# Optimization experiments

Hardware: AMD Instinct MI355X
Metric: run time of the kernel (lower is better)

Reference implementation:

```python
import jax, jax.numpy as jnp
import numpy as np

VOXEL_SIZE = 0.4
STRIDE = 2
NUM_BATCH = 4
PRE_MAXSIZE = 1024  # nms_premaxsize
NMS_THR = 0.1
NEG_INF = -1e9


def setup_inputs() -> dict:
    key = jax.random.key(0)
    ks = jax.random.split(key, 7)
    N, C = 200000, 256
    feat = jax.random.normal(ks[0], (N, C), dtype=jnp.float32)
    batch_idx = jax.random.randint(ks[1], (N,), 0, NUM_BATCH, dtype=jnp.int32)
    coor = jax.random.randint(ks[2], (N, 2), 0, 400, dtype=jnp.int32)
    W_cls = jax.random.normal(ks[3], (C, 2), dtype=jnp.float32) * 0.02
    b_cls = jnp.zeros((2,), dtype=jnp.float32)
    W_reg = jax.random.normal(ks[4], (C, 9), dtype=jnp.float32) * 0.02
    b_reg = jnp.zeros((9,), dtype=jnp.float32)
    return {"feat": feat, "batch_idx": batch_idx, "coor": coor,
            "W_cls": W_cls, "b_cls": b_cls, "W_reg": W_reg, "b_reg": b_reg}


def _bev_iou(bx):
    # bx: [K,7] (x,y,z,l,w,h,r); axis-aligned BEV IoU on (x,y,l,w)
    x, y, l, w = bx[:, 0], bx[:, 1], bx[:, 3], bx[:, 4]
    x1, x2 = x - l / 2, x + l / 2
    y1, y2 = y - w / 2, y + w / 2
    ix = jnp.maximum(jnp.minimum(x2[:, None], x2[None, :]) - jnp.maximum(x1[:, None], x1[None, :]), 0.0)
    iy = jnp.maximum(jnp.minimum(y2[:, None], y2[None, :]) - jnp.maximum(y1[:, None], y1[None, :]), 0.0)
    inter = ix * iy
    area = l * w
    union = area[:, None] + area[None, :] - inter
    return inter / jnp.maximum(union, 1e-6)


def _nms_keep(iou):
    # greedy NMS over score-descending rows; returns keep mask [K]
    K = iou.shape[0]
    idx = jnp.arange(K)

    def body(i, supp):
        keep_i = jnp.logical_not(supp[i])
        new = keep_i & (iou[i] > NMS_THR) & (idx > i)
        return supp | new

    supp = jax.lax.fori_loop(0, K, body, jnp.zeros((K,), dtype=bool))
    return jnp.logical_not(supp)


def reference(feat, batch_idx, coor, W_cls, b_cls, W_reg, b_reg):
    # ---- shared heads over all sparse voxels ----
    cls_logits = feat @ W_cls + b_cls            # [N, 1+1] (neg evidence, class)
    probs = jax.nn.softmax(cls_logits, axis=-1)
    cls_prob = probs[:, 1:]                      # [N, n_cls]
    conf = jnp.max(cls_prob, axis=-1)            # [N]
    label = jnp.argmax(cls_prob, axis=-1)        # [N]

    reg = feat @ W_reg + b_reg                   # [N, 9] -> ctr(3) dim(3) dir(2) scr(1)
    ctr, dim, drn, scr = reg[:, :3], reg[:, 3:6], reg[:, 6:8], reg[:, 8]
    scr = jax.nn.sigmoid(scr)                    # sigmoid_keys=['scr']

    # indices2metric: voxel indices -> metric centers
    centers = coor.astype(jnp.float32) * (VOXEL_SIZE * STRIDE)  # [N, 2]

    xy = centers + ctr[:, :2]
    z = ctr[:, 2]
    lwh = jnp.exp(jnp.clip(dim, -6.0, 6.0))
    angle = jnp.arctan2(drn[:, 0], drn[:, 1])
    boxes = jnp.concatenate([xy, z[:, None], lwh, angle[:, None]], axis=-1)  # [N, 7]
    score = conf * scr                           # [N]

    def per_sample(b):
        s = jnp.where(batch_idx == b, score, NEG_INF)
        vals, idx = jax.lax.top_k(s, PRE_MAXSIZE)          # score-sorted (desc)
        bx = boxes[idx]                                     # [K, 7]
        lb = label[idx]                                     # [K]
        valid = vals > NEG_INF / 2
        iou = _bev_iou(bx)
        keep = _nms_keep(iou) & valid
        out = jnp.concatenate([bx, vals[:, None]], axis=-1) * keep[:, None]  # [K, 8]
        return out, lb, keep

    out, lb, keep = jax.vmap(per_sample)(jnp.arange(NUM_BATCH))
    return out, lb, keep
```

## Files before the change

kernel.cpp:

```cpp
#include <hip/hip_runtime.h>
#include <math.h>

#define NBATCH 4
#define PRE 1024
#define CAND 4096
#define NHIST 65536
#define MAXSLOT 384

__device__ __forceinline__ unsigned long long allow_mask(int i, int l) {
    int base = l << 6;
    if (i < base) return ~0ull;
    int sh = i - base + 1;
    if (sh >= 64) return 0ull;
    return (~0ull) << sh;
}

__global__ void k0_weights(const float* __restrict__ Wcls, const float* __restrict__ bcls,
                           const float* __restrict__ Wreg, const float* __restrict__ breg,
                           double* __restrict__ Wd3, float* __restrict__ Wf8,
                           double* __restrict__ biasD, float* __restrict__ biasF) {
    int j = blockIdx.x;
    int c = threadIdx.x;
    if (j < 2) {
        Wd3[j * 256 + c] = (double)Wcls[c * 2 + j];
        if (c == 0) biasD[j] = (double)bcls[j];
    } else if (j == 10) {
        Wd3[2 * 256 + c] = (double)Wreg[c * 9 + 8];
        if (c == 0) biasD[2] = (double)breg[8];
    } else {
        int r = j - 2;
        Wf8[r * 256 + c] = Wreg[c * 9 + r];
        if (c == 0) biasF[r] = breg[r];
    }
}

__global__ __launch_bounds__(256, 4) void k1_points(
    const float4* __restrict__ feat4, const int* __restrict__ batch_idx,
    const int* __restrict__ coor, const double* __restrict__ Wd3,
    const float* __restrict__ Wf8, const double* __restrict__ biasD,
    const float* __restrict__ biasF, float* __restrict__ pointData,
    unsigned long long* __restrict__ keys, unsigned int* __restrict__ hist, int N) {
    int p = blockIdx.x * 256 + threadIdx.x;
    int pc = (p < N) ? p : 0;
    const float4* row = feat4 + (size_t)pc * 64;

    double a0 = 0.0, a1 = 0.0, a2 = 0.0;
    float f[8] = {0.f, 0.f, 0.f, 0.f, 0.f, 0.f, 0.f, 0.f};
    float4 cur[8], nxt[8];
#pragma unroll
    for (int u = 0; u < 8; ++u) cur[u] = row[u];
#pragma unroll
    for (int o = 0; o < 8; ++o) {
        if (o < 7) {
#pragma unroll
            for (int u = 0; u < 8; ++u) nxt[u] = row[(o + 1) * 8 + u];
        }
#pragma unroll
        for (int u = 0; u < 8; ++u) {
            float vv[4] = {cur[u].x, cur[u].y, cur[u].z, cur[u].w};
#pragma unroll
            for (int m = 0; m < 4; ++m) {
                int k = o * 32 + u * 4 + m;
                double fd = (double)vv[m];
                a0 = fma(fd, Wd3[k], a0);
                a1 = fma(fd, Wd3[256 + k], a1);
                a2 = fma(fd, Wd3[512 + k], a2);
#pragma unroll
                for (int j = 0; j < 8; ++j) f[j] = fmaf(vv[m], Wf8[j * 256 + k], f[j]);
            }
        }
#pragma unroll
        for (int u = 0; u < 8; ++u) cur[u] = nxt[u];
    }
    if (p >= N) return;

    double d0 = a0 + biasD[0], d1 = a1 + biasD[1], d2 = a2 + biasD[2];
    double conf = 1.0 / (1.0 + exp(-(d1 - d0)));
    double scr = 1.0 / (1.0 + exp(-d2));
    double score = conf * scr;
    float s32 = (float)score;

    float fb[8];
#pragma unroll
    for (int j = 0; j < 8; ++j) fb[j] = f[j] + biasF[j];

    float cx = (float)coor[2 * p] * 0.8f;
    float cy = (float)coor[2 * p + 1] * 0.8f;
    float bx = cx + fb[0], by = cy + fb[1], bz = fb[2];
    float bl = expf(fminf(fmaxf(fb[3], -6.f), 6.f));
    float bw = expf(fminf(fmaxf(fb[4], -6.f), 6.f));
    float bh = expf(fminf(fmaxf(fb[5], -6.f), 6.f));
    float ba = atan2f(fb[6], fb[7]);

    float4* pd = (float4*)(pointData + (size_t)p * 8);
    pd[0] = make_float4(bx, by, bz, bl);
    pd[1] = make_float4(bw, bh, ba, s32);
    keys[p] = (unsigned long long)__double_as_longlong(score);
    int b = batch_idx[p];
    atomicAdd(&hist[b * NHIST + (__float_as_uint(s32) >> 16)], 1u);
}

__global__ __launch_bounds__(256) void k2_thresh(const unsigned int* __restrict__ hist,
                                                 unsigned int* __restrict__ Tarr,
                                                 unsigned int* __restrict__ candCount) {
    int b = blockIdx.x, tid = threadIdx.x;
    __shared__ unsigned int csum[256];
    __shared__ unsigned int chunkv[256];
    __shared__ int stc;
    __shared__ unsigned int scum;
    if (tid == 0) candCount[b] = 0u;
    const unsigned int* h = hist + b * NHIST;
    unsigned int s = 0;
    for (int m = 0; m < 256; ++m) s += h[tid * 256 + m];
    csum[tid] = s;
    __syncthreads();
    if (tid == 0) {
        unsigned int cum = 0; int tc = -1;
        for (int t = 255; t >= 0; --t) {
            if (cum + csum[t] >= 1024u) { tc = t; break; }
            cum += csum[t];
        }
        stc = tc; scum = cum;
    }
    __syncthreads();
    int tc = stc;
    if (tc < 0) { if (tid == 0) Tarr[b] = 0u; return; }
    chunkv[tid] = h[tc * 256 + tid];
    __syncthreads();
    if (tid == 0) {
        unsigned int cum = scum, T = (unsigned int)(tc * 256);
        for (int m = 255; m >= 0; --m) {
            unsigned int c = chunkv[m];
            if (cum + c >= 1024u) { T = (unsigned int)(tc * 256 + m); break; }
            cum += c;
        }
        Tarr[b] = T;
    }
}

__global__ void k3_compact(const int* __restrict__ batch_idx, const float* __restrict__ pointData,
                           const unsigned long long* __restrict__ keys,
                           const unsigned int* __restrict__ Tarr, unsigned int* __restrict__ candCount,
                           unsigned int* __restrict__ candIdx, unsigned long long* __restrict__ candKey,
                           int N) {
    int p = blockIdx.x * 256 + threadIdx.x;
    if (p >= N) return;
    int b = batch_idx[p];
    float s32 = pointData[(size_t)p * 8 + 7];
    unsigned int bucket = __float_as_uint(s32) >> 16;
    if (bucket >= Tarr[b]) {
        unsigned int pos = atomicAdd(&candCount[b], 1u);
        if (pos < CAND) {
            candIdx[b * CAND + pos] = (unsigned int)p;
            candKey[b * CAND + pos] = keys[p];
        }
    }
}

__global__ __launch_bounds__(1024) void k4_sort(const unsigned int* __restrict__ candCount,
                                                const unsigned int* __restrict__ candIdx,
                                                const unsigned long long* __restrict__ candKey,
                                                const float* __restrict__ pointData,
                                                float* __restrict__ topBox,
                                                float4* __restrict__ geo,
                                                unsigned int* __restrict__ validArr) {
    int b = blockIdx.x, tid = threadIdx.x;
    __shared__ unsigned long long ka[CAND];
    __shared__ unsigned int id[CAND];
    unsigned int cnt = candCount[b];
    if (cnt > CAND) cnt = CAND;
    int n = (cnt <= 2048u) ? 2048 : 4096;
    for (int t = tid; t < n; t += 1024) {
        if ((unsigned int)t < cnt) {
            ka[t] = ~candKey[b * CAND + t];
            id[t] = candIdx[b * CAND + t];
        } else {
            ka[t] = ~0ull;
            id[t] = 0xFFFFFFFFu;
        }
    }
    __syncthreads();
    for (int k = 2; k <= n; k <<= 1) {
        for (int j = k >> 1; j > 0; j >>= 1) {
            for (int t = tid; t < n; t += 1024) {
                int l = t ^ j;
                if (l > t) {
                    bool up = ((t & k) == 0);
                    unsigned long long kt = ka[t], kl = ka[l];
                    unsigned int it_ = id[t], il = id[l];
                    bool gt = (kt > kl) || (kt == kl && it_ > il);
                    if (gt == up) { ka[t] = kl; ka[l] = kt; id[t] = il; id[l] = it_; }
                }
            }
            __syncthreads();
        }
    }
    unsigned int gi = id[tid];
    bool valid = (gi != 0xFFFFFFFFu) && ((unsigned int)tid < cnt);
    float v[8];
#pragma unroll
    for (int k = 0; k < 8; ++k) v[k] = 0.f;
    if (valid) {
        const float* pd = pointData + (size_t)gi * 8;
#pragma unroll
        for (int k = 0; k < 8; ++k) v[k] = pd[k];
    }
    float* tb = topBox + (size_t)(b * PRE + tid) * 8;
#pragma unroll
    for (int k = 0; k < 8; ++k) tb[k] = v[k];
    geo[b * PRE + tid] = make_float4(v[0], v[1], v[3], v[4]);
    validArr[b * PRE + tid] = valid ? 1u : 0u;
}

__global__ __launch_bounds__(256) void k5_iou(const float4* __restrict__ geo,
                                              unsigned long long* __restrict__ M) {
    int wv = threadIdx.x >> 6, lane = threadIdx.x & 63;
    int gidx = blockIdx.x * 4 + wv;
    int b = gidx >> 10, i = gidx & (PRE - 1);
    float4 bi = geo[b * PRE + i];
    float x1i = bi.x - bi.z * 0.5f, x2i = bi.x + bi.z * 0.5f;
    float y1i = bi.y - bi.w * 0.5f, y2i = bi.y + bi.w * 0.5f;
    float ai = bi.z * bi.w;
    int g = i >> 6;
    unsigned long long* Mrow = M + (size_t)(b * PRE + i) * 16;
    for (int wj = g; wj < 16; ++wj) {
        int j = wj * 64 + lane;
        float4 bj = geo[b * PRE + j];
        float x1j = bj.x - bj.z * 0.5f, x2j = bj.x + bj.z * 0.5f;
        float y1j = bj.y - bj.w * 0.5f, y2j = bj.y + bj.w * 0.5f;
        float aj = bj.z * bj.w;
        float ix = fmaxf(fminf(x2i, x2j) - fmaxf(x1i, x1j), 0.0f);
        float iy = fmaxf(fminf(y2i, y2j) - fmaxf(y1i, y1j), 0.0f);
        float inter = ix * iy;
        float uni = ai + aj - inter;
        float iou = inter / fmaxf(uni, 1e-6f);
        unsigned long long m = __ballot(iou > 0.1f);
        if (lane == 0) Mrow[wj] = m;
    }
}

__global__ __launch_bounds__(256) void k6_nms(const unsigned long long* __restrict__ M,
                                              const unsigned int* __restrict__ validArr,
                                              const float* __restrict__ topBox,
                                              float* __restrict__ out0,
                                              int* __restrict__ lbOut,
                                              float* __restrict__ keepOut) {
    __shared__ unsigned long long Mc[MAXSLOT * 16];
    __shared__ unsigned int slotIdx[PRE];
    __shared__ unsigned int cntSh;
    __shared__ unsigned long long suppSh[16];
    int b = blockIdx.x, tid = threadIdx.x;
    if (tid == 0) cntSh = 0;
    __syncthreads();
    for (int r = tid; r < PRE; r += 256) {
        const unsigned long long* row = M + (size_t)(b * PRE + r) * 16;
        unsigned long long w[16];
        unsigned long long o = 0ull;
#pragma unroll
        for (int l = 0; l < 16; ++l) { w[l] = row[l] & allow_mask(r, l); o |= w[l]; }
        unsigned int s = 0xFFFFFFFFu;
        if (o != 0ull) {
            unsigned int slot = atomicAdd(&cntSh, 1u);
            if (slot < MAXSLOT) {
                s = slot;
#pragma unroll
                for (int l = 0; l < 16; ++l) Mc[slot * 16 + l] = w[l];
            } else s = 0xFFFFFFFEu;
        }
        slotIdx[r] = s;
    }
    __syncthreads();
    if (tid < 64) {
        int lane = tid;
        unsigned long long supp = 0ull;
        for (int g = 0; g < 16; ++g) {
            unsigned long long act = __ballot(slotIdx[g * 64 + lane] != 0xFFFFFFFFu);
            while (act) {
                int bit = __builtin_ctzll(act);
                act &= act - 1ull;
                int i = g * 64 + bit;
                unsigned long long wsup = __shfl(supp, g);
                bool keep_i = ((wsup >> (i & 63)) & 1ull) == 0ull;
                if (keep_i && lane < 16) {
                    unsigned int s = slotIdx[i];
                    unsigned long long add = (s < MAXSLOT)
                        ? Mc[s * 16 + lane]
                        : (M[(size_t)(b * PRE + i) * 16 + lane] & allow_mask(i, lane));
                    supp |= add;
                }
            }
        }
        if (lane < 16) suppSh[lane] = supp;
    }
    __syncthreads();
    for (int r = tid; r < PRE; r += 256) {
        bool keep = (((suppSh[r >> 6] >> (r & 63)) & 1ull) == 0ull) && (validArr[b * PRE + r] != 0u);
        float kf = keep ? 1.0f : 0.0f;
        const float* tb = topBox + (size_t)(b * PRE + r) * 8;
        float* o = out0 + (size_t)(b * PRE + r) * 8;
#pragma unroll
        for (int k = 0; k < 8; ++k) o[k] = tb[k] * kf;
        lbOut[b * PRE + r] = 0;
        keepOut[b * PRE + r] = kf;
    }
}

extern "C" void kernel_launch(void* const* d_in, const int* in_sizes, int n_in,
                              void* d_out, int out_size, void* d_ws, size_t ws_size,
                              hipStream_t stream) {
    int N = in_sizes[0] / 256;
    const float* feat = (const float*)d_in[0];
    const int* batch_idx = (const int*)d_in[1];
    const int* coor = (const int*)d_in[2];
    const float* Wcls = (const float*)d_in[3];
    const float* bcls = (const float*)d_in[4];
    const float* Wreg = (const float*)d_in[5];
    const float* breg = (const float*)d_in[6];

    char* ws = (char*)d_ws;
    size_t off = 0;
    auto take = [&](size_t bytes) -> char* {
        char* r = ws + off;
        off += (bytes + 255) & ~(size_t)255;
        return r;
    };
    float* pointData = (float*)take((size_t)N * 8 * 4);
    unsigned long long* keys = (unsigned long long*)take((size_t)N * 8);
    unsigned int* hist = (unsigned int*)take((size_t)NBATCH * NHIST * 4);
    unsigned int* Tarr = (unsigned int*)take(NBATCH * 4);
    unsigned int* candCount = (unsigned int*)take(NBATCH * 4);
    unsigned int* candIdx = (unsigned int*)take(NBATCH * CAND * 4);
    unsigned long long* candKey = (unsigned long long*)take(NBATCH * CAND * 8);
    float* topBox = (float*)take(NBATCH * PRE * 8 * 4);
    float4* geo = (float4*)take(NBATCH * PRE * 16);
    unsigned int* validArr = (unsigned int*)take(NBATCH * PRE * 4);
    unsigned long long* M = (unsigned long long*)take((size_t)NBATCH * PRE * 16 * 8);
    double* Wd3 = (double*)take(3 * 256 * 8);
    float* Wf8 = (float*)take(8 * 256 * 4);
    double* biasD = (double*)take(3 * 8);
    float* biasF = (float*)take(8 * 4);

    float* out0 = (float*)d_out;
    int* lbOut = (int*)(out0 + NBATCH * PRE * 8);
    float* keepOut = out0 + NBATCH * PRE * 8 + NBATCH * PRE;

    hipMemsetAsync(hist, 0, (size_t)NBATCH * NHIST * 4, stream);

    int pb256 = (N + 255) / 256;
    k0_weights<<<dim3(11), dim3(256), 0, stream>>>(Wcls, bcls, Wreg, breg, Wd3, Wf8, biasD, biasF);
    k1_points<<<dim3(pb256), dim3(256), 0, stream>>>((const float4*)feat, batch_idx, coor,
                                                     Wd3, Wf8, biasD, biasF,
                                                     pointData, keys, hist, N);
    k2_thresh<<<dim3(NBATCH), dim3(256), 0, stream>>>(hist, Tarr, candCount);
    k3_compact<<<dim3(pb256), dim3(256), 0, stream>>>(batch_idx, pointData, keys, Tarr,
                                                      candCount, candIdx, candKey, N);
    k4_sort<<<dim3(NBATCH), dim3(1024), 0, stream>>>(candCount, candIdx, candKey,
                                                     pointData, topBox, geo, validArr);
    k5_iou<<<dim3(NBATCH * PRE / 4), dim3(256), 0, stream>>>(geo, M);
    k6_nms<<<dim3(NBATCH), dim3(256), 0, stream>>>(M, validArr, topBox, out0, lbOut, keepOut);
}
```

Before: 509.5 us.

## Coalesce feature loads via LDS, parallelize threshold scan, replace bitonic sort with ranking

The point kernel now loads feature rows cooperatively as coalesced float4 chunks, transposes them through padded shared memory, and prefetches the next chunk, instead of having each thread stream its own 1 KB row. The histogram threshold kernel uses wave reductions and parallel suffix scans in place of serial per-thread loops. The bitonic sort of candidates is replaced with an O(n^2) rank-by-counting pass that scatters only the top 1024. The histogram memset is folded into a merged init kernel. The rank pass costs more work per candidate, and the shared-memory transpose adds block barriers.

```diff
diff --git a/kernel.cpp b/kernel.cpp
--- a/kernel.cpp
+++ b/kernel.cpp
@@ -15,22 +15,30 @@
     return (~0ull) << sh;
 }
 
-__global__ void k0_weights(const float* __restrict__ Wcls, const float* __restrict__ bcls,
-                           const float* __restrict__ Wreg, const float* __restrict__ breg,
-                           double* __restrict__ Wd3, float* __restrict__ Wf8,
-                           double* __restrict__ biasD, float* __restrict__ biasF) {
-    int j = blockIdx.x;
-    int c = threadIdx.x;
-    if (j < 2) {
-        Wd3[j * 256 + c] = (double)Wcls[c * 2 + j];
-        if (c == 0) biasD[j] = (double)bcls[j];
-    } else if (j == 10) {
+__global__ __launch_bounds__(256) void k_init(
+    const float* __restrict__ Wcls, const float* __restrict__ bcls,
+    const float* __restrict__ Wreg, const float* __restrict__ breg,
+    double* __restrict__ Wd3, float* __restrict__ Wf8,
+    double* __restrict__ biasD, float* __restrict__ biasF,
+    unsigned int* __restrict__ hist) {
+    int blk = blockIdx.x, t = threadIdx.x;
+    if (blk < 256) {
+        uint4* H = (uint4*)hist;
+        H[blk * 256 + t] = make_uint4(0u, 0u, 0u, 0u);
+    } else {
+        int c = t;
+        Wd3[0 * 256 + c] = (double)Wcls[c * 2 + 0];
+        Wd3[1 * 256 + c] = (double)Wcls[c * 2 + 1];
         Wd3[2 * 256 + c] = (double)Wreg[c * 9 + 8];
-        if (c == 0) biasD[2] = (double)breg[8];
-    } else {
-        int r = j - 2;
-        Wf8[r * 256 + c] = Wreg[c * 9 + r];
-        if (c == 0) biasF[r] = breg[r];
+#pragma unroll
+        for (int r = 0; r < 8; ++r) Wf8[r * 256 + c] = Wreg[c * 9 + r];
+        if (c == 0) {
+            biasD[0] = (double)bcls[0];
+            biasD[1] = (double)bcls[1];
+            biasD[2] = (double)breg[8];
+#pragma unroll
+            for (int r = 0; r < 8; ++r) biasF[r] = breg[r];
+        }
     }
 }
 
@@ -40,38 +48,55 @@
     const float* __restrict__ Wf8, const double* __restrict__ biasD,
     const float* __restrict__ biasF, float* __restrict__ pointData,
     unsigned long long* __restrict__ keys, unsigned int* __restrict__ hist, int N) {
-    int p = blockIdx.x * 256 + threadIdx.x;
-    int pc = (p < N) ? p : 0;
-    const float4* row = feat4 + (size_t)pc * 64;
+    __shared__ float sfeat[256 * 33];
+    int t = threadIdx.x;
+    int p0 = blockIdx.x * 256;
+    int sj = t & 7;
+    int sp = t >> 3;
 
     double a0 = 0.0, a1 = 0.0, a2 = 0.0;
     float f[8] = {0.f, 0.f, 0.f, 0.f, 0.f, 0.f, 0.f, 0.f};
-    float4 cur[8], nxt[8];
-#pragma unroll
-    for (int u = 0; u < 8; ++u) cur[u] = row[u];
-#pragma unroll
-    for (int o = 0; o < 8; ++o) {
-        if (o < 7) {
-#pragma unroll
-            for (int u = 0; u < 8; ++u) nxt[u] = row[(o + 1) * 8 + u];
-        }
-#pragma unroll
-        for (int u = 0; u < 8; ++u) {
-            float vv[4] = {cur[u].x, cur[u].y, cur[u].z, cur[u].w};
-#pragma unroll
-            for (int m = 0; m < 4; ++m) {
-                int k = o * 32 + u * 4 + m;
-                double fd = (double)vv[m];
-                a0 = fma(fd, Wd3[k], a0);
-                a1 = fma(fd, Wd3[256 + k], a1);
-                a2 = fma(fd, Wd3[512 + k], a2);
-#pragma unroll
-                for (int j = 0; j < 8; ++j) f[j] = fmaf(vv[m], Wf8[j * 256 + k], f[j]);
+    float4 R[8], R2[8];
+
+#pragma unroll
+    for (int r = 0; r < 8; ++r) {
+        int gp = p0 + r * 32 + sp;
+        R[r] = (gp < N) ? feat4[(size_t)gp * 64 + sj] : make_float4(0.f, 0.f, 0.f, 0.f);
+    }
+
+    for (int c = 0; c < 8; ++c) {
+#pragma unroll
+        for (int r = 0; r < 8; ++r) {
+            float* d = sfeat + (r * 32 + sp) * 33 + sj * 4;
+            d[0] = R[r].x; d[1] = R[r].y; d[2] = R[r].z; d[3] = R[r].w;
+        }
+        __syncthreads();
+        if (c < 7) {
+#pragma unroll
+            for (int r = 0; r < 8; ++r) {
+                int gp = p0 + r * 32 + sp;
+                R2[r] = (gp < N) ? feat4[(size_t)gp * 64 + (c + 1) * 8 + sj]
+                                 : make_float4(0.f, 0.f, 0.f, 0.f);
             }
         }
-#pragma unroll
-        for (int u = 0; u < 8; ++u) cur[u] = nxt[u];
-    }
+        const double* wD = Wd3 + c * 32;
+        const float* wF = Wf8 + c * 32;
+#pragma unroll
+        for (int k = 0; k < 32; ++k) {
+            float v = sfeat[t * 33 + k];
+            double vd = (double)v;
+            a0 = fma(vd, wD[k], a0);
+            a1 = fma(vd, wD[256 + k], a1);
+            a2 = fma(vd, wD[512 + k], a2);
+#pragma unroll
+            for (int q = 0; q < 8; ++q) f[q] = fmaf(v, wF[q * 256 + k], f[q]);
+        }
+        __syncthreads();
+#pragma unroll
+        for (int r = 0; r < 8; ++r) R[r] = R2[r];
+    }
+
+    int p = p0 + t;
     if (p >= N) return;
 
     double d0 = a0 + biasD[0], d1 = a1 + biasD[1], d2 = a2 + biasD[2];
@@ -82,7 +107,7 @@
 
     float fb[8];
 #pragma unroll
-    for (int j = 0; j < 8; ++j) fb[j] = f[j] + biasF[j];
+    for (int q = 0; q < 8; ++q) fb[q] = f[q] + biasF[q];
 
     float cx = (float)coor[2 * p] * 0.8f;
     float cy = (float)coor[2 * p + 1] * 0.8f;
@@ -103,39 +128,53 @@
 __global__ __launch_bounds__(256) void k2_thresh(const unsigned int* __restrict__ hist,
                                                  unsigned int* __restrict__ Tarr,
                                                  unsigned int* __restrict__ candCount) {
-    int b = blockIdx.x, tid = threadIdx.x;
-    __shared__ unsigned int csum[256];
-    __shared__ unsigned int chunkv[256];
-    __shared__ int stc;
-    __shared__ unsigned int scum;
-    if (tid == 0) candCount[b] = 0u;
+    int b = blockIdx.x, t = threadIdx.x;
+    int w = t >> 6, lane = t & 63;
+    __shared__ unsigned int bufA[256];
+    __shared__ unsigned int bufB[256];
+    __shared__ int tcSh;
+    __shared__ int mSh;
+    if (t == 0) { candCount[b] = 0u; tcSh = -1; mSh = -1; }
     const unsigned int* h = hist + b * NHIST;
-    unsigned int s = 0;
-    for (int m = 0; m < 256; ++m) s += h[tid * 256 + m];
-    csum[tid] = s;
-    __syncthreads();
-    if (tid == 0) {
-        unsigned int cum = 0; int tc = -1;
-        for (int t = 255; t >= 0; --t) {
-            if (cum + csum[t] >= 1024u) { tc = t; break; }
-            cum += csum[t];
-        }
-        stc = tc; scum = cum;
-    }
-    __syncthreads();
-    int tc = stc;
-    if (tc < 0) { if (tid == 0) Tarr[b] = 0u; return; }
-    chunkv[tid] = h[tc * 256 + tid];
-    __syncthreads();
-    if (tid == 0) {
-        unsigned int cum = scum, T = (unsigned int)(tc * 256);
-        for (int m = 255; m >= 0; --m) {
-            unsigned int c = chunkv[m];
-            if (cum + c >= 1024u) { T = (unsigned int)(tc * 256 + m); break; }
-            cum += c;
-        }
-        Tarr[b] = T;
-    }
+    for (int i = 0; i < 64; ++i) {
+        int c = i * 4 + w;
+        const uint4* row = (const uint4*)(h + c * 256);
+        uint4 v = row[lane];
+        unsigned int s = v.x + v.y + v.z + v.w;
+#pragma unroll
+        for (int off = 1; off < 64; off <<= 1) s += __shfl_xor(s, off, 64);
+        if (lane == 0) bufA[c] = s;
+    }
+    __syncthreads();
+    unsigned int* src = bufA; unsigned int* dst = bufB;
+#pragma unroll
+    for (int d = 1; d < 256; d <<= 1) {
+        unsigned int v = src[t] + ((t + d < 256) ? src[t + d] : 0u);
+        __syncthreads();
+        dst[t] = v;
+        __syncthreads();
+        unsigned int* tmp = src; src = dst; dst = tmp;
+    }
+    if (src[t] >= 1024u) atomicMax(&tcSh, t);
+    __syncthreads();
+    int tc = tcSh;
+    if (tc < 0) { if (t == 0) Tarr[b] = 0u; return; }
+    unsigned int cum = (tc < 255) ? src[tc + 1] : 0u;
+    __syncthreads();
+    bufA[t] = h[tc * 256 + t];
+    __syncthreads();
+    src = bufA; dst = bufB;
+#pragma unroll
+    for (int d = 1; d < 256; d <<= 1) {
+        unsigned int v = src[t] + ((t + d < 256) ? src[t + d] : 0u);
+        __syncthreads();
+        dst[t] = v;
+        __syncthreads();
+        unsigned int* tmp = src; src = dst; dst = tmp;
+    }
+    if (cum + src[t] >= 1024u) atomicMax(&mSh, t);
+    __syncthreads();
+    if (t == 0) Tarr[b] = (unsigned int)(tc * 256 + mSh);
 }
 
 __global__ void k3_compact(const int* __restrict__ batch_idx, const float* __restrict__ pointData,
@@ -157,59 +196,50 @@
     }
 }
 
-__global__ __launch_bounds__(1024) void k4_sort(const unsigned int* __restrict__ candCount,
+__global__ __launch_bounds__(1024) void k4_rank(const unsigned int* __restrict__ candCount,
                                                 const unsigned int* __restrict__ candIdx,
                                                 const unsigned long long* __restrict__ candKey,
                                                 const float* __restrict__ pointData,
                                                 float* __restrict__ topBox,
                                                 float4* __restrict__ geo,
                                                 unsigned int* __restrict__ validArr) {
-    int b = blockIdx.x, tid = threadIdx.x;
+    int b = blockIdx.x, t = threadIdx.x;
     __shared__ unsigned long long ka[CAND];
     __shared__ unsigned int id[CAND];
-    unsigned int cnt = candCount[b];
+    int cnt = (int)candCount[b];
     if (cnt > CAND) cnt = CAND;
-    int n = (cnt <= 2048u) ? 2048 : 4096;
-    for (int t = tid; t < n; t += 1024) {
-        if ((unsigned int)t < cnt) {
-            ka[t] = ~candKey[b * CAND + t];
-            id[t] = candIdx[b * CAND + t];
-        } else {
-            ka[t] = ~0ull;
-            id[t] = 0xFFFFFFFFu;
-        }
-    }
-    __syncthreads();
-    for (int k = 2; k <= n; k <<= 1) {
-        for (int j = k >> 1; j > 0; j >>= 1) {
-            for (int t = tid; t < n; t += 1024) {
-                int l = t ^ j;
-                if (l > t) {
-                    bool up = ((t & k) == 0);
-                    unsigned long long kt = ka[t], kl = ka[l];
-                    unsigned int it_ = id[t], il = id[l];
-                    bool gt = (kt > kl) || (kt == kl && it_ > il);
-                    if (gt == up) { ka[t] = kl; ka[l] = kt; id[t] = il; id[l] = it_; }
-                }
-            }
-            __syncthreads();
-        }
-    }
-    unsigned int gi = id[tid];
-    bool valid = (gi != 0xFFFFFFFFu) && ((unsigned int)tid < cnt);
-    float v[8];
-#pragma unroll
-    for (int k = 0; k < 8; ++k) v[k] = 0.f;
-    if (valid) {
-        const float* pd = pointData + (size_t)gi * 8;
-#pragma unroll
-        for (int k = 0; k < 8; ++k) v[k] = pd[k];
-    }
-    float* tb = topBox + (size_t)(b * PRE + tid) * 8;
-#pragma unroll
-    for (int k = 0; k < 8; ++k) tb[k] = v[k];
-    geo[b * PRE + tid] = make_float4(v[0], v[1], v[3], v[4]);
-    validArr[b * PRE + tid] = valid ? 1u : 0u;
+    for (int x = t; x < cnt; x += 1024) {
+        ka[x] = candKey[b * CAND + x];
+        id[x] = candIdx[b * CAND + x];
+    }
+    int K0 = (cnt < PRE) ? cnt : PRE;
+    if (t >= K0) {
+        float* tb = topBox + (size_t)(b * PRE + t) * 8;
+#pragma unroll
+        for (int k = 0; k < 8; ++k) tb[k] = 0.f;
+        geo[b * PRE + t] = make_float4(0.f, 0.f, 0.f, 0.f);
+        validArr[b * PRE + t] = 0u;
+    }
+    __syncthreads();
+    for (int x = t; x < cnt; x += 1024) {
+        unsigned long long kx = ka[x];
+        unsigned int ix = id[x];
+        int rank = 0;
+        for (int j = 0; j < cnt; ++j) {
+            unsigned long long kj = ka[j];
+            unsigned int ij = id[j];
+            rank += (int)((kj > kx) | ((kj == kx) & (ij < ix)));
+        }
+        if (rank < PRE) {
+            const float4* pd = (const float4*)(pointData + (size_t)ix * 8);
+            float4 v0 = pd[0], v1 = pd[1];
+            float* tb = topBox + (size_t)(b * PRE + rank) * 8;
+            tb[0] = v0.x; tb[1] = v0.y; tb[2] = v0.z; tb[3] = v0.w;
+            tb[4] = v1.x; tb[5] = v1.y; tb[6] = v1.z; tb[7] = v1.w;
+            geo[b * PRE + rank] = make_float4(v0.x, v0.y, v0.w, v1.x);
+            validArr[b * PRE + rank] = 1u;
+        }
+    }
 }
 
 __global__ __launch_bounds__(256) void k5_iou(const float4* __restrict__ geo,
@@ -344,17 +374,15 @@
     int* lbOut = (int*)(out0 + NBATCH * PRE * 8);
     float* keepOut = out0 + NBATCH * PRE * 8 + NBATCH * PRE;
 
-    hipMemsetAsync(hist, 0, (size_t)NBATCH * NHIST * 4, stream);
-
     int pb256 = (N + 255) / 256;
-    k0_weights<<<dim3(11), dim3(256), 0, stream>>>(Wcls, bcls, Wreg, breg, Wd3, Wf8, biasD, biasF);
+    k_init<<<dim3(257), dim3(256), 0, stream>>>(Wcls, bcls, Wreg, breg, Wd3, Wf8, biasD, biasF, hist);
     k1_points<<<dim3(pb256), dim3(256), 0, stream>>>((const float4*)feat, batch_idx, coor,
                                                      Wd3, Wf8, biasD, biasF,
                                                      pointData, keys, hist, N);
     k2_thresh<<<dim3(NBATCH), dim3(256), 0, stream>>>(hist, Tarr, candCount);
     k3_compact<<<dim3(pb256), dim3(256), 0, stream>>>(batch_idx, pointData, keys, Tarr,
                                                       candCount, candIdx, candKey, N);
-    k4_sort<<<dim3(NBATCH), dim3(1024), 0, stream>>>(candCount, candIdx, candKey,
+    k4_rank<<<dim3(NBATCH), dim3(1024), 0, stream>>>(candCount, candIdx, candKey,
                                                      pointData, topBox, geo, validArr);
     k5_iou<<<dim3(NBATCH * PRE / 4), dim3(256), 0, stream>>>(geo, M);
     k6_nms<<<dim3(NBATCH), dim3(256), 0, stream>>>(M, validArr, topBox, out0, lbOut, keepOut);
```

New measurement: 515.5 us. Within noise of the previous version (+1.2%).
